# Optimization experiments

Measured on AMD Instinct MI355X. Metric: run time of the kernel, lower is better.

Reference implementation:

```python
import jax, jax.numpy as jnp
import numpy as np

K = 3
STRIDE = 1
PAD = 1
DIL = 1


def conv2d(x, w, b, stride, pad, dil):
    y = jax.lax.conv_general_dilated(
        x, w, (stride, stride), [(pad, pad), (pad, pad)],
        rhs_dilation=(dil, dil), dimension_numbers=("NCHW", "OIHW", "NCHW"))
    return y + b[None, :, None, None]


def bilinear_gather(img, ys, xs):
    # img: (C,H,W); ys,xs: (KK,Ho,Wo) pixel coords.
    # grid_sample(mode=bilinear, padding_mode=zeros, align_corners=True):
    # out-of-range corners contribute 0, interpolation weights unchanged.
    H, W = img.shape[-2:]
    y0 = jnp.floor(ys)
    x0 = jnp.floor(xs)
    wy1 = ys - y0
    wx1 = xs - x0
    wy0 = 1.0 - wy1
    wx0 = 1.0 - wx1

    def g(yc, xc):
        yi = yc.astype(jnp.int32)
        xi = xc.astype(jnp.int32)
        valid = (yi >= 0) & (yi < H) & (xi >= 0) & (xi < W)
        yi = jnp.clip(yi, 0, H - 1)
        xi = jnp.clip(xi, 0, W - 1)
        v = img[:, yi, xi]  # (C,KK,Ho,Wo)
        return v * valid[None].astype(img.dtype)

    return (g(y0, x0) * (wy0 * wx0)[None]
            + g(y0, x0 + 1.0) * (wy0 * wx1)[None]
            + g(y0 + 1.0, x0) * (wy1 * wx0)[None]
            + g(y0 + 1.0, x0 + 1.0) * (wy1 * wx1)[None])


def setup_inputs() -> dict:
    key = jax.random.key(0)
    ks = jax.random.split(key, 4)
    B, C_in, H, W = 8, 64, 96, 96
    C_out = 64
    x = jax.random.normal(ks[0], (B, C_in, H, W), dtype=jnp.float32)
    weight = jax.random.normal(ks[1], (C_out, C_in, K, K), dtype=jnp.float32) * 0.05
    bias = jax.random.normal(ks[2], (C_out,), dtype=jnp.float32) * 0.01
    off_w = jax.random.normal(ks[3], (2 * K * K, C_in, K, K), dtype=jnp.float32) * 0.05
    off_b = jnp.zeros((2 * K * K,), dtype=jnp.float32)
    return {"x": x, "weight": weight, "bias": bias, "off_w": off_w, "off_b": off_b}


def reference(x, weight, bias, off_w, off_b):
    B, C, H, W = x.shape
    Ho = (H + 2 * PAD - DIL * (K - 1) - 1) // STRIDE + 1
    Wo = (W + 2 * PAD - DIL * (K - 1) - 1) // STRIDE + 1

    offsets = conv2d(x, off_w, off_b, STRIDE, PAD, DIL)  # (B,2*K*K,Ho,Wo)
    off = offsets.reshape(B, K * K, 2, Ho, Wo)

    # Base sampling grid (note: original code does NOT subtract padding; kept faithful).
    by, bx = jnp.meshgrid(jnp.arange(Ho, dtype=x.dtype), jnp.arange(Wo, dtype=x.dtype), indexing="ij")
    by = by * STRIDE + (K // 2) * DIL
    bx = bx * STRIDE + (K // 2) * DIL
    ko = jnp.arange(-(K // 2), K // 2 + 1, dtype=x.dtype)
    ky, kx = jnp.meshgrid(ko, ko, indexing="ij")

    sy = by[None, None] + ky.reshape(1, -1, 1, 1) + off[:, :, 0]  # (B,KK,Ho,Wo)
    sx = bx[None, None] + kx.reshape(1, -1, 1, 1) + off[:, :, 1]

    sampled = jax.vmap(bilinear_gather)(x, sy, sx)  # (B,C,KK,Ho,Wo)

    wflat = weight.reshape(weight.shape[0], C, K * K)  # (O,C,KK)
    out = jnp.einsum("bckhw,ock->bohw", sampled, wflat)
    return out + bias[None, :, None, None]
```

## Files before the change

kernel.cpp:

```cpp
#include <hip/hip_runtime.h>
#include <hip/hip_bf16.h>

#define HH 96
#define WW 96
#define HW 9216
#define NB 8

typedef __bf16 bf16x8 __attribute__((ext_vector_type(8)));
typedef float  f32x4  __attribute__((ext_vector_type(4)));

union BF8 { uint4 u; bf16x8 v; unsigned short s[8]; };

__device__ __forceinline__ unsigned short f2bf_bits(float f) {
    unsigned u = __float_as_uint(f);
    unsigned r = u + 0x7FFFu + ((u >> 16) & 1u);
    return (unsigned short)(r >> 16);
}
__device__ __forceinline__ float bf2f(unsigned short s) {
    return __uint_as_float(((unsigned)s) << 16);
}
__device__ __forceinline__ unsigned pkbf(float a, float b) {
    union { __hip_bfloat162 h; unsigned u; } c;
    c.h = __float22bfloat162_rn(make_float2(a, b));
    return c.u;
}

__device__ __forceinline__ void bl_setup(int h, int w, int r, int s, float oy, float ox,
                                         int* a, float* wg) {
    float sy = (float)(h + r) + oy;
    float sx = (float)(w + s) + ox;
    float fy = floorf(sy), fx = floorf(sx);
    int   y0 = (int)fy, x0 = (int)fx;
    int   y1 = y0 + 1, x1 = x0 + 1;
    float wy1 = sy - fy, wx1 = sx - fx;
    float wy0 = 1.f - wy1, wx0 = 1.f - wx1;
    float m00 = (y0 >= 0 && y0 < HH && x0 >= 0 && x0 < WW) ? 1.f : 0.f;
    float m01 = (y0 >= 0 && y0 < HH && x1 >= 0 && x1 < WW) ? 1.f : 0.f;
    float m10 = (y1 >= 0 && y1 < HH && x0 >= 0 && x0 < WW) ? 1.f : 0.f;
    float m11 = (y1 >= 0 && y1 < HH && x1 >= 0 && x1 < WW) ? 1.f : 0.f;
    int cy0 = min(max(y0, 0), HH - 1), cy1 = min(max(y1, 0), HH - 1);
    int cx0 = min(max(x0, 0), WW - 1), cx1 = min(max(x1, 0), WW - 1);
    a[0] = (cy0 * WW + cx0) * 64;  a[1] = (cy0 * WW + cx1) * 64;
    a[2] = (cy1 * WW + cx0) * 64;  a[3] = (cy1 * WW + cx1) * 64;
    wg[0] = wy0 * wx0 * m00;  wg[1] = wy0 * wx1 * m01;
    wg[2] = wy1 * wx0 * m10;  wg[3] = wy1 * wx1 * m11;
}

__global__ __launch_bounds__(256) void xcvt_prep(const float* __restrict__ x,
                                                 const float* __restrict__ weight,
                                                 const float* __restrict__ off_w,
                                                 unsigned short* __restrict__ xt,
                                                 unsigned short* __restrict__ wTb,
                                                 unsigned short* __restrict__ owTb) {
    __shared__ unsigned short T[64 * 64];
    int bid   = blockIdx.x;
    int t     = threadIdx.x;
    int b     = bid & 7;
    int pbase = (bid >> 3) * 64;
    int pl    = t & 63;
    int q     = t >> 6;

    const float* xp = x + ((size_t)(b * 64 + q * 16)) * HW + pbase + pl;
    unsigned short hb[16];
#pragma unroll
    for (int i = 0; i < 16; ++i) hb[i] = f2bf_bits(xp[(size_t)i * HW]);

    uint4 w0, w1;
    w0.x = hb[0]  | (hb[1]  << 16); w0.y = hb[2]  | (hb[3]  << 16);
    w0.z = hb[4]  | (hb[5]  << 16); w0.w = hb[6]  | (hb[7]  << 16);
    w1.x = hb[8]  | (hb[9]  << 16); w1.y = hb[10] | (hb[11] << 16);
    w1.z = hb[12] | (hb[13] << 16); w1.w = hb[14] | (hb[15] << 16);
    int sw = pl & 7;
    *(uint4*)&T[pl * 64 + (((2 * q)     ^ sw) << 3)] = w0;
    *(uint4*)&T[pl * 64 + (((2 * q + 1) ^ sw) << 3)] = w1;
    __syncthreads();

    int row = t >> 2, rs = row & 7;
    uint4 a  = *(const uint4*)&T[row * 64 + ((((t & 3) * 2)     ^ rs) << 3)];
    uint4 b2 = *(const uint4*)&T[row * 64 + ((((t & 3) * 2 + 1) ^ rs) << 3)];
    unsigned short* dst = xt + ((size_t)(b * HW + pbase)) * 64 + t * 16;
    *(uint4*)dst       = a;
    *(uint4*)(dst + 8) = b2;

    if (bid < 216) {
        int i = bid * 256 + t;
        if (i < 36864) {
            int tap = i >> 12;
            int co  = (i >> 6) & 63;
            int c   = i & 63;
            wTb[i] = f2bf_bits(weight[(co * 64 + c) * 9 + tap]);
        } else {
            int f   = i - 36864;
            int j   = f / 576;
            int kk  = f - j * 576;
            int tap = kk >> 6;
            int c   = kk & 63;
            owTb[f] = (j < 18) ? f2bf_bits(off_w[(j * 64 + c) * 9 + tap]) : (unsigned short)0;
        }
    }
}

__global__ __launch_bounds__(256) void deform_all(const unsigned short* __restrict__ xt,
                                                  const unsigned short* __restrict__ wTb,
                                                  const unsigned short* __restrict__ owTb,
                                                  const float* __restrict__ bias,
                                                  const float* __restrict__ ob,
                                                  float* __restrict__ out) {
    __shared__ unsigned short S[2][64 * 64];
    __shared__ float offs[64 * 20];

    int bid   = blockIdx.x;
    int t     = threadIdx.x;
    int b     = bid & 7;
    int pbase = (bid >> 3) * 64;

    int e    = t & 7;
    int base = t >> 3;
    int px0  = pbase + base;
    int px1  = px0 + 32;
    int h0 = px0 / WW, w0 = px0 - h0 * WW;
    int h1 = px1 / WW, w1 = px1 - h1 * WW;
    int sw = base & 7;

    int ln = t & 15;
    int qd = (t >> 4) & 3;
    int wv = t >> 6;

    const unsigned short* xb = xt + (size_t)b * HW * 64;

    f32x4 accj[2] = {{0.f, 0.f, 0.f, 0.f}, {0.f, 0.f, 0.f, 0.f}};

    for (int tap = 0; tap < 9; ++tap) {
        int cur = tap & 1;
        int r = tap / 3, s = tap - r * 3;

        int  iy0 = h0 - 1 + r, ix0 = w0 - 1 + s;
        bool v0  = (iy0 >= 0) & (iy0 < HH) & (ix0 >= 0) & (ix0 < WW);
        int  a0  = (min(max(iy0, 0), HH - 1) * WW + min(max(ix0, 0), WW - 1)) * 64;
        int  iy1 = h1 - 1 + r, ix1 = w1 - 1 + s;
        bool v1  = (iy1 >= 0) & (iy1 < HH) & (ix1 >= 0) & (ix1 < WW);
        int  a1  = (min(max(iy1, 0), HH - 1) * WW + min(max(ix1, 0), WW - 1)) * 64;

        uint4 p0 = *(const uint4*)(xb + a0 + e * 8);
        uint4 p1 = *(const uint4*)(xb + a1 + e * 8);
        if (!v0) p0 = make_uint4(0, 0, 0, 0);
        if (!v1) p1 = make_uint4(0, 0, 0, 0);
        *(uint4*)&S[cur][base * 64 + ((e ^ sw) << 3)]        = p0;
        *(uint4*)&S[cur][(base + 32) * 64 + ((e ^ sw) << 3)] = p1;
        __syncthreads();

        int  row = wv * 16 + ln, rs = row & 7;
        BF8  fa0, fa1;
        fa0.u = *(const uint4*)&S[cur][row * 64 + ((qd       ^ rs) << 3)];
        fa1.u = *(const uint4*)&S[cur][row * 64 + (((qd + 4) ^ rs) << 3)];
#pragma unroll
        for (int jt = 0; jt < 2; ++jt) {
            const unsigned short* brow = owTb + (size_t)(jt * 16 + ln) * 576 + tap * 64 + qd * 8;
            BF8 fb0, fb1;
            fb0.u = *(const uint4*)brow;
            fb1.u = *(const uint4*)(brow + 32);
            accj[jt] = __builtin_amdgcn_mfma_f32_16x16x32_bf16(fa0.v, fb0.v, accj[jt], 0, 0, 0);
            accj[jt] = __builtin_amdgcn_mfma_f32_16x16x32_bf16(fa1.v, fb1.v, accj[jt], 0, 0, 0);
        }
    }

    {
        int   rowp = wv * 16 + qd * 4;
        float obj = ob[ln];
#pragma unroll
        for (int rg = 0; rg < 4; ++rg) offs[(rowp + rg) * 20 + ln] = accj[0][rg] + obj;
        if (ln < 2) {
            float obj1 = ob[16 + ln];
#pragma unroll
            for (int rg = 0; rg < 4; ++rg) offs[(rowp + rg) * 20 + 16 + ln] = accj[1][rg] + obj1;
        }
    }
    __syncthreads();

    f32x4 acc[4] = {{0.f,0.f,0.f,0.f},{0.f,0.f,0.f,0.f},{0.f,0.f,0.f,0.f},{0.f,0.f,0.f,0.f}};

    for (int tap = 0; tap < 9; ++tap) {
        int cur = tap & 1;
        int r = tap / 3, s = tap - r * 3;

        float oy0 = offs[base * 20 + 2 * tap],        ox0 = offs[base * 20 + 2 * tap + 1];
        float oy1 = offs[(base + 32) * 20 + 2 * tap], ox1 = offs[(base + 32) * 20 + 2 * tap + 1];

        int   a0[4], a1[4];
        float g0[4], g1[4];
        bl_setup(h0, w0, r, s, oy0, ox0, a0, g0);
        bl_setup(h1, w1, r, s, oy1, ox1, a1, g1);

        uint4 cA[4], cB[4];
#pragma unroll
        for (int c = 0; c < 4; ++c) cA[c] = *(const uint4*)(xb + a0[c] + e * 8);
#pragma unroll
        for (int c = 0; c < 4; ++c) cB[c] = *(const uint4*)(xb + a1[c] + e * 8);

        {
            BF8 q0, q1, q2, q3;
            q0.u = cA[0]; q1.u = cA[1]; q2.u = cA[2]; q3.u = cA[3];
            float v[8];
#pragma unroll
            for (int i = 0; i < 8; ++i)
                v[i] = g0[0] * bf2f(q0.s[i]) + g0[1] * bf2f(q1.s[i])
                     + g0[2] * bf2f(q2.s[i]) + g0[3] * bf2f(q3.s[i]);
            uint4 sv;
            sv.x = pkbf(v[0], v[1]); sv.y = pkbf(v[2], v[3]);
            sv.z = pkbf(v[4], v[5]); sv.w = pkbf(v[6], v[7]);
            *(uint4*)&S[cur][base * 64 + ((e ^ sw) << 3)] = sv;
        }
        {
            BF8 q0, q1, q2, q3;
            q0.u = cB[0]; q1.u = cB[1]; q2.u = cB[2]; q3.u = cB[3];
            float v[8];
#pragma unroll
            for (int i = 0; i < 8; ++i)
                v[i] = g1[0] * bf2f(q0.s[i]) + g1[1] * bf2f(q1.s[i])
                     + g1[2] * bf2f(q2.s[i]) + g1[3] * bf2f(q3.s[i]);
            uint4 sv;
            sv.x = pkbf(v[0], v[1]); sv.y = pkbf(v[2], v[3]);
            sv.z = pkbf(v[4], v[5]); sv.w = pkbf(v[6], v[7]);
            *(uint4*)&S[cur][(base + 32) * 64 + ((e ^ sw) << 3)] = sv;
        }
        __syncthreads();

        {
            const unsigned short* wb = wTb + (size_t)tap * 4096 + (wv * 16 + ln) * 64 + qd * 8;
            BF8 fb0, fb1;
            fb0.u = *(const uint4*)wb;
            fb1.u = *(const uint4*)(wb + 32);
#pragma unroll
            for (int pt = 0; pt < 4; ++pt) {
                int row = pt * 16 + ln, rs = row & 7;
                BF8 fa0, fa1;
                fa0.u = *(const uint4*)&S[cur][row * 64 + ((qd       ^ rs) << 3)];
                fa1.u = *(const uint4*)&S[cur][row * 64 + (((qd + 4) ^ rs) << 3)];
                acc[pt] = __builtin_amdgcn_mfma_f32_16x16x32_bf16(fa0.v, fb0.v, acc[pt], 0, 0, 0);
                acc[pt] = __builtin_amdgcn_mfma_f32_16x16x32_bf16(fa1.v, fb1.v, acc[pt], 0, 0, 0);
            }
        }
    }

    int   co = wv * 16 + ln;
    float bv = bias[co];
    float* ob2 = out + ((size_t)(b * 64 + co)) * HW + pbase + qd * 4;
#pragma unroll
    for (int pt = 0; pt < 4; ++pt) {
        float4 st;
        st.x = acc[pt].x + bv; st.y = acc[pt].y + bv;
        st.z = acc[pt].z + bv; st.w = acc[pt].w + bv;
        *(float4*)(ob2 + pt * 16) = st;
    }
}

extern "C" void kernel_launch(void* const* d_in, const int* in_sizes, int n_in,
                              void* d_out, int out_size, void* d_ws, size_t ws_size,
                              hipStream_t stream) {
    const float* x      = (const float*)d_in[0];
    const float* weight = (const float*)d_in[1];
    const float* bias   = (const float*)d_in[2];
    const float* off_w  = (const float*)d_in[3];
    const float* off_b  = (const float*)d_in[4];
    float* out = (float*)d_out;

    unsigned short* xt   = (unsigned short*)d_ws;
    unsigned short* wTb  = xt + 4718592;
    unsigned short* owTb = wTb + 36864;

    hipLaunchKernelGGL(xcvt_prep,  dim3(1152), dim3(256), 0, stream,
                       x, weight, off_w, xt, wTb, owTb);
    hipLaunchKernelGGL(deform_all, dim3(1152), dim3(256), 0, stream,
                       xt, wTb, owTb, bias, off_b, out);
}
```

Before: 132.5 us.

## Halve pixel tile per block and redistribute offset-conv MFMA across waves

Each block now handles 32 pixels instead of 64, launching twice as many blocks. The offset-conv MFMA work is split so each wave computes one 16x16 tile rather than two, and per-pixel offsets are preloaded into registers before the deformable loop. Smaller tiles cut registers and LDS per block, which should raise occupancy and latency hiding for the gather loads. The cost is more blocks, more barriers per pixel, and weight fragments reloaded twice as often.

```diff
diff --git a/kernel.cpp b/kernel.cpp
--- a/kernel.cpp
+++ b/kernel.cpp
@@ -106,21 +106,19 @@
                                                   const float* __restrict__ bias,
                                                   const float* __restrict__ ob,
                                                   float* __restrict__ out) {
-    __shared__ unsigned short S[2][64 * 64];
-    __shared__ float offs[64 * 20];
+    __shared__ unsigned short S[2][32 * 64];
+    __shared__ float offs[32 * 20];
 
     int bid   = blockIdx.x;
     int t     = threadIdx.x;
     int b     = bid & 7;
-    int pbase = (bid >> 3) * 64;
-
-    int e    = t & 7;
-    int base = t >> 3;
-    int px0  = pbase + base;
-    int px1  = px0 + 32;
-    int h0 = px0 / WW, w0 = px0 - h0 * WW;
-    int h1 = px1 / WW, w1 = px1 - h1 * WW;
-    int sw = base & 7;
+    int pbase = (bid >> 3) * 32;
+
+    int e   = t & 7;
+    int pxl = t >> 3;
+    int px  = pbase + pxl;
+    int h   = px / WW, w = px - h * WW;
+    int sw  = pxl & 7;
 
     int ln = t & 15;
     int qd = (t >> 4) & 3;
@@ -128,101 +126,75 @@
 
     const unsigned short* xb = xt + (size_t)b * HW * 64;
 
-    f32x4 accj[2] = {{0.f, 0.f, 0.f, 0.f}, {0.f, 0.f, 0.f, 0.f}};
+    int ptA = wv & 1, jtA = wv >> 1;
+    f32x4 accj = {0.f, 0.f, 0.f, 0.f};
 
     for (int tap = 0; tap < 9; ++tap) {
         int cur = tap & 1;
         int r = tap / 3, s = tap - r * 3;
 
-        int  iy0 = h0 - 1 + r, ix0 = w0 - 1 + s;
-        bool v0  = (iy0 >= 0) & (iy0 < HH) & (ix0 >= 0) & (ix0 < WW);
-        int  a0  = (min(max(iy0, 0), HH - 1) * WW + min(max(ix0, 0), WW - 1)) * 64;
-        int  iy1 = h1 - 1 + r, ix1 = w1 - 1 + s;
-        bool v1  = (iy1 >= 0) & (iy1 < HH) & (ix1 >= 0) & (ix1 < WW);
-        int  a1  = (min(max(iy1, 0), HH - 1) * WW + min(max(ix1, 0), WW - 1)) * 64;
-
-        uint4 p0 = *(const uint4*)(xb + a0 + e * 8);
-        uint4 p1 = *(const uint4*)(xb + a1 + e * 8);
-        if (!v0) p0 = make_uint4(0, 0, 0, 0);
-        if (!v1) p1 = make_uint4(0, 0, 0, 0);
-        *(uint4*)&S[cur][base * 64 + ((e ^ sw) << 3)]        = p0;
-        *(uint4*)&S[cur][(base + 32) * 64 + ((e ^ sw) << 3)] = p1;
+        int  iy = h - 1 + r, ix = w - 1 + s;
+        bool vd = (iy >= 0) & (iy < HH) & (ix >= 0) & (ix < WW);
+        int  ad = (min(max(iy, 0), HH - 1) * WW + min(max(ix, 0), WW - 1)) * 64;
+        uint4 p = *(const uint4*)(xb + ad + e * 8);
+        if (!vd) p = make_uint4(0, 0, 0, 0);
+        *(uint4*)&S[cur][pxl * 64 + ((e ^ sw) << 3)] = p;
         __syncthreads();
 
-        int  row = wv * 16 + ln, rs = row & 7;
-        BF8  fa0, fa1;
+        int  row = ptA * 16 + ln, rs = row & 7;
+        BF8  fa0, fa1, fb0, fb1;
         fa0.u = *(const uint4*)&S[cur][row * 64 + ((qd       ^ rs) << 3)];
         fa1.u = *(const uint4*)&S[cur][row * 64 + (((qd + 4) ^ rs) << 3)];
-#pragma unroll
-        for (int jt = 0; jt < 2; ++jt) {
-            const unsigned short* brow = owTb + (size_t)(jt * 16 + ln) * 576 + tap * 64 + qd * 8;
-            BF8 fb0, fb1;
-            fb0.u = *(const uint4*)brow;
-            fb1.u = *(const uint4*)(brow + 32);
-            accj[jt] = __builtin_amdgcn_mfma_f32_16x16x32_bf16(fa0.v, fb0.v, accj[jt], 0, 0, 0);
-            accj[jt] = __builtin_amdgcn_mfma_f32_16x16x32_bf16(fa1.v, fb1.v, accj[jt], 0, 0, 0);
+        const unsigned short* brow = owTb + (size_t)(jtA * 16 + ln) * 576 + tap * 64 + qd * 8;
+        fb0.u = *(const uint4*)brow;
+        fb1.u = *(const uint4*)(brow + 32);
+        accj = __builtin_amdgcn_mfma_f32_16x16x32_bf16(fa0.v, fb0.v, accj, 0, 0, 0);
+        accj = __builtin_amdgcn_mfma_f32_16x16x32_bf16(fa1.v, fb1.v, accj, 0, 0, 0);
+    }
+
+    {
+        int j = jtA * 16 + ln;
+        if (j < 18) {
+            int   rowp = ptA * 16 + qd * 4;
+            float obj  = ob[j];
+#pragma unroll
+            for (int rg = 0; rg < 4; ++rg) offs[(rowp + rg) * 20 + j] = accj[rg] + obj;
         }
     }
-
-    {
-        int   rowp = wv * 16 + qd * 4;
-        float obj = ob[ln];
-#pragma unroll
-        for (int rg = 0; rg < 4; ++rg) offs[(rowp + rg) * 20 + ln] = accj[0][rg] + obj;
-        if (ln < 2) {
-            float obj1 = ob[16 + ln];
-#pragma unroll
-            for (int rg = 0; rg < 4; ++rg) offs[(rowp + rg) * 20 + 16 + ln] = accj[1][rg] + obj1;
-        }
-    }
     __syncthreads();
 
-    f32x4 acc[4] = {{0.f,0.f,0.f,0.f},{0.f,0.f,0.f,0.f},{0.f,0.f,0.f,0.f},{0.f,0.f,0.f,0.f}};
+    float oy[9], ox[9];
+#pragma unroll
+    for (int k = 0; k < 9; ++k) {
+        float2 p = *(const float2*)&offs[pxl * 20 + 2 * k];
+        oy[k] = p.x; ox[k] = p.y;
+    }
+
+    f32x4 acc[2] = {{0.f,0.f,0.f,0.f},{0.f,0.f,0.f,0.f}};
 
     for (int tap = 0; tap < 9; ++tap) {
         int cur = tap & 1;
         int r = tap / 3, s = tap - r * 3;
 
-        float oy0 = offs[base * 20 + 2 * tap],        ox0 = offs[base * 20 + 2 * tap + 1];
-        float oy1 = offs[(base + 32) * 20 + 2 * tap], ox1 = offs[(base + 32) * 20 + 2 * tap + 1];
-
-        int   a0[4], a1[4];
-        float g0[4], g1[4];
-        bl_setup(h0, w0, r, s, oy0, ox0, a0, g0);
-        bl_setup(h1, w1, r, s, oy1, ox1, a1, g1);
-
-        uint4 cA[4], cB[4];
-#pragma unroll
-        for (int c = 0; c < 4; ++c) cA[c] = *(const uint4*)(xb + a0[c] + e * 8);
-#pragma unroll
-        for (int c = 0; c < 4; ++c) cB[c] = *(const uint4*)(xb + a1[c] + e * 8);
-
-        {
-            BF8 q0, q1, q2, q3;
-            q0.u = cA[0]; q1.u = cA[1]; q2.u = cA[2]; q3.u = cA[3];
-            float v[8];
-#pragma unroll
-            for (int i = 0; i < 8; ++i)
-                v[i] = g0[0] * bf2f(q0.s[i]) + g0[1] * bf2f(q1.s[i])
-                     + g0[2] * bf2f(q2.s[i]) + g0[3] * bf2f(q3.s[i]);
-            uint4 sv;
-            sv.x = pkbf(v[0], v[1]); sv.y = pkbf(v[2], v[3]);
-            sv.z = pkbf(v[4], v[5]); sv.w = pkbf(v[6], v[7]);
-            *(uint4*)&S[cur][base * 64 + ((e ^ sw) << 3)] = sv;
-        }
-        {
-            BF8 q0, q1, q2, q3;
-            q0.u = cB[0]; q1.u = cB[1]; q2.u = cB[2]; q3.u = cB[3];
-            float v[8];
-#pragma unroll
-            for (int i = 0; i < 8; ++i)
-                v[i] = g1[0] * bf2f(q0.s[i]) + g1[1] * bf2f(q1.s[i])
-                     + g1[2] * bf2f(q2.s[i]) + g1[3] * bf2f(q3.s[i]);
-            uint4 sv;
-            sv.x = pkbf(v[0], v[1]); sv.y = pkbf(v[2], v[3]);
-            sv.z = pkbf(v[4], v[5]); sv.w = pkbf(v[6], v[7]);
-            *(uint4*)&S[cur][(base + 32) * 64 + ((e ^ sw) << 3)] = sv;
-        }
+        int   a[4];
+        float g[4];
+        bl_setup(h, w, r, s, oy[tap], ox[tap], a, g);
+
+        uint4 cA[4];
+#pragma unroll
+        for (int c = 0; c < 4; ++c) cA[c] = *(const uint4*)(xb + a[c] + e * 8);
+
+        BF8 q0, q1, q2, q3;
+        q0.u = cA[0]; q1.u = cA[1]; q2.u = cA[2]; q3.u = cA[3];
+        float v[8];
+#pragma unroll
+        for (int i = 0; i < 8; ++i)
+            v[i] = g[0] * bf2f(q0.s[i]) + g[1] * bf2f(q1.s[i])
+                 + g[2] * bf2f(q2.s[i]) + g[3] * bf2f(q3.s[i]);
+        uint4 sv;
+        sv.x = pkbf(v[0], v[1]); sv.y = pkbf(v[2], v[3]);
+        sv.z = pkbf(v[4], v[5]); sv.w = pkbf(v[6], v[7]);
+        *(uint4*)&S[cur][pxl * 64 + ((e ^ sw) << 3)] = sv;
         __syncthreads();
 
         {
@@ -231,7 +203,7 @@
             fb0.u = *(const uint4*)wb;
             fb1.u = *(const uint4*)(wb + 32);
 #pragma unroll
-            for (int pt = 0; pt < 4; ++pt) {
+            for (int pt = 0; pt < 2; ++pt) {
                 int row = pt * 16 + ln, rs = row & 7;
                 BF8 fa0, fa1;
                 fa0.u = *(const uint4*)&S[cur][row * 64 + ((qd       ^ rs) << 3)];
@@ -246,7 +218,7 @@
     float bv = bias[co];
     float* ob2 = out + ((size_t)(b * 64 + co)) * HW + pbase + qd * 4;
 #pragma unroll
-    for (int pt = 0; pt < 4; ++pt) {
+    for (int pt = 0; pt < 2; ++pt) {
         float4 st;
         st.x = acc[pt].x + bv; st.y = acc[pt].y + bv;
         st.z = acc[pt].z + bv; st.w = acc[pt].w + bv;
@@ -270,6 +242,6 @@
 
     hipLaunchKernelGGL(xcvt_prep,  dim3(1152), dim3(256), 0, stream,
                        x, weight, off_w, xt, wTb, owTb);
-    hipLaunchKernelGGL(deform_all, dim3(1152), dim3(256), 0, stream,
+    hipLaunchKernelGGL(deform_all, dim3(2304), dim3(256), 0, stream,
                        xt, wTb, owTb, bias, off_b, out);
 }
```

New measurement: 136.1 us. 1.03x slower.
